# Performance work log

Measured on AMD Instinct MI355X. Metric: run time of the kernel, lower is better.

Reference implementation:

```python
import jax, jax.numpy as jnp
import numpy as np

HIDDEN = 1024
NUM_HEADS = 16
HEAD_DIM = HIDDEN // NUM_HEADS
EPS = 1e-12


def _layernorm(x, g, b):
    mu = jnp.mean(x, axis=-1, keepdims=True)
    var = jnp.var(x, axis=-1, keepdims=True)
    return (x - mu) * jax.lax.rsqrt(var + EPS) * g + b


def _attention(q, k, v, mask, Wd, bd, ln_g, ln_b):
    # q: [B,T,H], k/v: [B,S,H], mask: [B,1,1,S] additive
    B, T, _ = q.shape
    S = k.shape[1]
    qh = q.reshape(B, T, NUM_HEADS, HEAD_DIM).transpose(0, 2, 1, 3)  # [B,h,T,d]
    kh = k.reshape(B, S, NUM_HEADS, HEAD_DIM).transpose(0, 2, 1, 3)
    vh = v.reshape(B, S, NUM_HEADS, HEAD_DIM).transpose(0, 2, 1, 3)
    scores = jnp.einsum('bhtd,bhsd->bhts', qh, kh) / jnp.sqrt(jnp.float32(HEAD_DIM))
    if mask is not None:
        scores = scores + mask
    probs = jax.nn.softmax(scores, axis=-1)  # dropout = identity in eval
    ctx = jnp.einsum('bhts,bhsd->bthd', probs, vh)  # [B,T,h,d]
    # torch: w = dense.weight.t().view(h, d, H); einsum('bfnd,ndh->bfh')
    w = Wd.T.reshape(NUM_HEADS, HEAD_DIM, HIDDEN)
    proj = jnp.einsum('bthd,hdH->btH', ctx, w) + bd
    # residual is the (projected) query tensor q, per source
    return _layernorm(q + proj, ln_g, ln_b)


def setup_inputs() -> dict:
    key = jax.random.key(0)
    ks = jax.random.split(key, 12)
    s = 0.02
    B, S, T = 4, 1024, 1024
    return {
        'encoder_states': jax.random.normal(ks[0], (B, S, HIDDEN), jnp.float32),
        'decoder_inputs': jax.random.normal(ks[1], (B, T, HIDDEN), jnp.float32),
        'src_attention_mask': jnp.zeros((B, 1, 1, S), jnp.float32),
        'tgt_attention_mask': jnp.zeros((B, 1, 1, T), jnp.float32),
        'Wq': jax.random.normal(ks[2], (HIDDEN, HIDDEN), jnp.float32) * s,
        'bq': jnp.zeros((HIDDEN,), jnp.float32),
        'Wk': jax.random.normal(ks[3], (HIDDEN, HIDDEN), jnp.float32) * s,
        'bk': jnp.zeros((HIDDEN,), jnp.float32),
        'Wv': jax.random.normal(ks[4], (HIDDEN, HIDDEN), jnp.float32) * s,
        'bv': jnp.zeros((HIDDEN,), jnp.float32),
        'Wd': jax.random.normal(ks[5], (HIDDEN, HIDDEN), jnp.float32) * s,
        'bd': jnp.zeros((HIDDEN,), jnp.float32),
        'ln_g': jnp.ones((HIDDEN,), jnp.float32),
        'ln_b': jnp.zeros((HIDDEN,), jnp.float32),
    }


def reference(encoder_states, decoder_inputs, src_attention_mask, tgt_attention_mask,
              Wq, bq, Wk, bk, Wv, bv, Wd, bd, ln_g, ln_b):
    # projections (torch Linear: x @ W.T + b)
    q1 = decoder_inputs @ Wq.T + bq
    k1 = decoder_inputs @ Wk.T + bk
    v1 = decoder_inputs @ Wv.T + bv
    ek = encoder_states @ Wk.T + bk
    ev = encoder_states @ Wv.T + bv
    # self-attention over decoder states
    self_out = _attention(q1, k1, v1, tgt_attention_mask, Wd, bd, ln_g, ln_b)
    # cross-attention: query = self_out directly (no extra projection, per source)
    out = _attention(self_out, ek, ev, src_attention_mask, Wd, bd, ln_g, ln_b)
    return out
```

## Files before the change

kernel.cpp:

```cpp
#include <hip/hip_runtime.h>
#include <stdint.h>


#define B_   4
#define T_   1024
#define S_   1024
#define H_   1024
#define LOG2E 1.44269504088896340736f
#define SCALE_K (0.125f * LOG2E)

typedef __attribute__((ext_vector_type(8)))  __bf16       bf16x8;
typedef __attribute__((ext_vector_type(4)))  float        f32x4;
typedef __attribute__((ext_vector_type(16))) float        f32x16;
typedef __attribute__((ext_vector_type(4)))  unsigned int uint4v;

static __device__ __forceinline__ float bf2f(unsigned int u) {
    return __builtin_bit_cast(float, u << 16);
}
static __device__ __forceinline__ unsigned short f2bf(float f) {
    unsigned int x = __builtin_bit_cast(unsigned int, f);
    return (unsigned short)((x + 0x7fffu + ((x >> 16) & 1u)) >> 16);
}
static __device__ __forceinline__ unsigned int cvt_pk_bf16(float lo, float hi) {
    unsigned int r;
    asm("v_cvt_pk_bf16_f32 %0, %1, %2" : "=v"(r) : "v"(lo), "v"(hi));
    return r;
}
static __device__ __forceinline__ void perm32swap(unsigned int& a, unsigned int& b) {
    asm("v_permlane32_swap_b32 %0, %1" : "+v"(a), "+v"(b));
}
static __device__ __forceinline__ f32x4 mfma16(bf16x8 a, bf16x8 b, f32x4 c) {
    return __builtin_amdgcn_mfma_f32_16x16x32_bf16(a, b, c, 0, 0, 0);
}
static __device__ __forceinline__ f32x16 mfma32(bf16x8 a, bf16x8 b, f32x16 c) {
    return __builtin_amdgcn_mfma_f32_32x32x16_bf16(a, b, c, 0, 0, 0);
}

typedef const __attribute__((address_space(1))) void gv_t;
typedef __attribute__((address_space(3))) void lv_t;
static __device__ __forceinline__ void g2lds16(const void* g, void* l) {
    __builtin_amdgcn_global_load_lds((gv_t*)(size_t)g, (lv_t*)(unsigned int)(size_t)l, 16, 0, 0);
}

struct CvtArgs {
    const float* src[6];
    unsigned short* dst[6];
    float scale[6];
    int n4[6];
};
__global__ __launch_bounds__(256)
void cvt_multi(CvtArgs a) {
    const int k = blockIdx.y;
    const int i = blockIdx.x * 256 + threadIdx.x;
    if (i >= a.n4[k]) return;
    const float s = a.scale[k];
    float4 v = ((const float4*)a.src[k])[i];
    uint2 o;
    o.x = (unsigned)f2bf(v.x * s) | ((unsigned)f2bf(v.y * s) << 16);
    o.y = (unsigned)f2bf(v.z * s) | ((unsigned)f2bf(v.w * s) << 16);
    ((uint2*)a.dst[k])[i] = o;
}

struct GemmJob {
    const unsigned short* A[5];
    const unsigned short* W[5];
    const float* bias[5];
    float bs[5];
    unsigned short* O[5];
};
__global__ __launch_bounds__(256, 2)
void gemm_bf16(GemmJob job)
{
    __shared__ char smem[32768];
    char* As = smem;
    char* Bs = smem + 16384;
    const int tid = threadIdx.x;
    const int lane = tid & 63;
    const int w = tid >> 6;
    const int c = lane & 15, g = lane >> 4;
    const int wm = (w >> 1) * 64, wn = (w & 1) * 64;
    const int m0 = blockIdx.x * 128;
    const int set = blockIdx.y >> 3;
    const int n0 = (blockIdx.y & 7) * 128;
    const unsigned short* A    = job.A[set];
    const unsigned short* W    = job.W[set];
    const float* bias          = job.bias[set];
    const float bscale         = job.bs[set];
    unsigned short* O          = job.O[set];

    f32x4 acc[4][4];
#pragma unroll
    for (int i = 0; i < 4; i++)
#pragma unroll
        for (int j = 0; j < 4; j++) acc[i][j] = (f32x4){0.f, 0.f, 0.f, 0.f};

    const int srow = w * 32 + (lane >> 3);
    const int swzc = ((lane & 7) ^ (lane >> 3)) * 8;
    const unsigned short* gA = A + (size_t)(m0 + srow) * 1024 + swzc;
    const unsigned short* gB = W + (size_t)(n0 + srow) * 1024 + swzc;
    char* lA = As + w * 4096;
    char* lB = Bs + w * 4096;

    for (int kk = 0; kk < 1024; kk += 64) {
#pragma unroll
        for (int q = 0; q < 4; q++) {
            g2lds16(gA + kk + q*8192, lA + q*1024);
            g2lds16(gB + kk + q*8192, lB + q*1024);
        }
        __syncthreads();
#pragma unroll
        for (int ksub = 0; ksub < 2; ksub++) {
            bf16x8 af[4], bfr[4];
#pragma unroll
            for (int t = 0; t < 4; t++) {
                const int ra = wm + t*16 + c;
                const int rb = wn + t*16 + c;
                const int so = ((ksub*4 + g) ^ (c & 7)) << 4;
                af[t]  = *(const bf16x8*)(As + ra*128 + so);
                bfr[t] = *(const bf16x8*)(Bs + rb*128 + so);
            }
#pragma unroll
            for (int i = 0; i < 4; i++)
#pragma unroll
                for (int j = 0; j < 4; j++)
                    acc[i][j] = mfma16(af[i], bfr[j], acc[i][j]);
        }
        __syncthreads();
    }

    float bvv[4];
#pragma unroll
    for (int j = 0; j < 4; j++) bvv[j] = bias[n0 + wn + j*16 + c] * bscale;
    char* eb = As + w * 4096;
#pragma unroll
    for (int p = 0; p < 2; p++) {
#pragma unroll
        for (int ii = 0; ii < 2; ii++) {
            const int i = p*2 + ii;
#pragma unroll
            for (int j = 0; j < 4; j++)
#pragma unroll
                for (int r = 0; r < 4; r++)
                    *(unsigned short*)(eb + (ii*16 + g*4 + r)*128 + (c + j*16)*2)
                        = f2bf(acc[i][j][r] + bvv[j]);
        }
        asm volatile("s_waitcnt lgkmcnt(0)" ::: "memory");
#pragma unroll
        for (int it = 0; it < 4; it++) {
            const int lrow = it*8 + (lane >> 3);
            uint4 vv = *(const uint4*)(eb + lrow*128 + (lane & 7)*16);
            *(uint4*)(O + (size_t)(m0 + wm + p*32 + lrow)*1024 + n0 + wn + (lane & 7)*8) = vv;
        }
        if (p == 0) asm volatile("s_waitcnt lgkmcnt(0)" ::: "memory");
    }
}

__global__ __launch_bounds__(256)
void transpose_v(const unsigned short* __restrict__ V, unsigned short* __restrict__ VT)
{
    __shared__ char sm[8192];
    const int tid = threadIdx.x;
    const int bh = blockIdx.y, b = bh >> 4, h = bh & 15;
    const int s0 = blockIdx.x * 64;
    for (int u = tid; u < 512; u += 256) {
        const int r = u >> 3, sg = u & 7;
        uint4 v = *(const uint4*)(V + (size_t)(b*S_ + s0 + r)*H_ + h*64 + sg*8);
        *(uint4*)(sm + r*128 + ((sg*16) ^ ((r & 7) << 4))) = v;
    }
    __syncthreads();
    const int d = tid >> 2, ss = tid & 3;
    unsigned int ow[8];
#pragma unroll
    for (int j2 = 0; j2 < 8; j2++) {
        const int s_a = ss*16 + 2*j2, s_b = s_a + 1;
        unsigned int ta = *(const unsigned short*)(sm + s_a*128 + ((2*d) ^ ((s_a & 7) << 4)));
        unsigned int tb = *(const unsigned short*)(sm + s_b*128 + ((2*d) ^ ((s_b & 7) << 4)));
        ow[j2] = ta | (tb << 16);
    }
    unsigned short* op = VT + (size_t)(bh*64 + d)*S_ + s0 + ss*16;
    uint4 o0, o1;
    o0.x = ow[0]; o0.y = ow[1]; o0.z = ow[2]; o0.w = ow[3];
    o1.x = ow[4]; o1.y = ow[5]; o1.z = ow[6]; o1.w = ow[7];
    *(uint4*)op = o0;
    *(uint4*)(op + 8) = o1;
}

__global__ __launch_bounds__(256, 4)
void attn_fused2(const unsigned short* __restrict__ Q,
                 const unsigned short* __restrict__ Kx,
                 const unsigned short* __restrict__ VT,
                 const float* __restrict__ mask,
                 unsigned short* __restrict__ Octx)
{
    __shared__ char smem[32768 + 4096 + 512 + 16];
    float* mb   = (float*)(smem + 32768);
    float* lbuf = (float*)(smem + 32768 + 4096);
    int* flag   = (int*)(smem + 32768 + 4096 + 512);

    const int tid = threadIdx.x;
    const int lane = tid & 63, w = tid >> 6;
    const int qc = lane & 31, hi = lane >> 5;
    const int bh = blockIdx.y, b = bh >> 4, h = bh & 15;
    const int q0 = blockIdx.x * 128 + w * 32;

    const int r0 = tid >> 3, sg = tid & 7;
    const unsigned short* gK0 = Kx + (size_t)(b*S_ + r0)*H_  + h*64 + sg*8;
    const unsigned short* gK1 = gK0 + (size_t)32*H_;
    const unsigned short* gV0 = VT + (size_t)(bh*64 + r0)*S_ + sg*8;
    const unsigned short* gV1 = gV0 + (size_t)32*S_;
    const int woff = r0*128 + ((sg*16) ^ ((r0 & 7) << 4));

    const unsigned short* qptr = Q + (size_t)(b*T_ + q0 + qc)*H_ + h*64 + hi*8;
    bf16x8 qf[4];
#pragma unroll
    for (int s = 0; s < 4; s++) qf[s] = *(const bf16x8*)(qptr + s*16);

    uint4 cK0 = *(const uint4*)gK0;
    uint4 cK1 = *(const uint4*)gK1;
    uint4 cV0 = *(const uint4*)gV0;
    uint4 cV1 = *(const uint4*)gV1;

    if (tid == 0) *flag = 0;
    __syncthreads();
    {
        float4 mv = ((const float4*)(mask + (size_t)b*S_))[tid];
        float4 ms;
        ms.x = mv.x * LOG2E; ms.y = mv.y * LOG2E; ms.z = mv.z * LOG2E; ms.w = mv.w * LOG2E;
        ((float4*)mb)[tid] = ms;
        if (mv.x != 0.f || mv.y != 0.f || mv.z != 0.f || mv.w != 0.f) atomicOr(flag, 1);
    }
    {
        char* b0 = smem;
        *(uint4*)(b0 + woff)               = cK0;
        *(uint4*)(b0 + 4096 + woff)        = cK1;
        *(uint4*)(b0 + 8192 + woff)        = cV0;
        *(uint4*)(b0 + 8192 + 4096 + woff) = cV1;
    }
    __syncthreads();
    const int msk = *flag;

    f32x16 o0 = {}, o1 = {};
    float lacc = 0.f;

    for (int t = 0; t < 16; ++t) {
        uint4 nK0, nK1, nV0, nV1;
        if (t < 15) {
            const size_t ko = (size_t)(t + 1) * 64 * H_;
            const int    vo = (t + 1) * 64;
            nK0 = *(const uint4*)(gK0 + ko);
            nK1 = *(const uint4*)(gK1 + ko);
            nV0 = *(const uint4*)(gV0 + vo);
            nV1 = *(const uint4*)(gV1 + vo);
        }
        char* Ks = smem + (t & 1) * 16384;
        char* Vs = Ks + 8192;

#pragma unroll
        for (int ts = 0; ts < 2; ++ts) {
            f32x16 st = {};
            __builtin_amdgcn_s_setprio(1);
#pragma unroll
            for (int step = 0; step < 4; ++step) {
                bf16x8 ak = *(const bf16x8*)(Ks + (ts*32 + qc)*128 +
                             ((step*32 + hi*16) ^ ((qc & 7) << 4)));
                st = mfma32(ak, qf[step], st);
            }
            __builtin_amdgcn_s_setprio(0);

            float pv[16];
            if (msk) {
#pragma unroll
                for (int rq = 0; rq < 4; ++rq) {
                    const float4 bb = *(const float4*)(mb + t*64 + ts*32 + rq*8 + hi*4);
#pragma unroll
                    for (int e = 0; e < 4; ++e)
                        pv[rq*4 + e] = __builtin_amdgcn_exp2f(st[rq*4 + e] + (&bb.x)[e]);
                }
            } else {
#pragma unroll
                for (int r = 0; r < 16; ++r) pv[r] = __builtin_amdgcn_exp2f(st[r]);
            }
#pragma unroll
            for (int r = 0; r < 16; ++r) lacc += pv[r];

#pragma unroll
            for (int half = 0; half < 2; ++half) {
                unsigned w0 = cvt_pk_bf16(pv[half*8 + 0], pv[half*8 + 1]);
                unsigned w1 = cvt_pk_bf16(pv[half*8 + 2], pv[half*8 + 3]);
                unsigned w2 = cvt_pk_bf16(pv[half*8 + 4], pv[half*8 + 5]);
                unsigned w3 = cvt_pk_bf16(pv[half*8 + 6], pv[half*8 + 7]);
                perm32swap(w0, w2);
                perm32swap(w1, w3);
                uint4v fw; fw[0] = w0; fw[1] = w1; fw[2] = w2; fw[3] = w3;
                const bf16x8 pa = __builtin_bit_cast(bf16x8, fw);
                const int scol = (ts*64 + half*32 + hi*16) ^ ((qc & 7) << 4);
                bf16x8 v0 = *(const bf16x8*)(Vs + qc*128        + scol);
                bf16x8 v1 = *(const bf16x8*)(Vs + (32 + qc)*128 + scol);
                __builtin_amdgcn_s_setprio(1);
                o0 = mfma32(pa, v0, o0);
                o1 = mfma32(pa, v1, o1);
                __builtin_amdgcn_s_setprio(0);
            }
        }

        if (t < 15) {
            char* nxt = smem + ((t + 1) & 1) * 16384;
            *(uint4*)(nxt + woff)               = nK0;
            *(uint4*)(nxt + 4096 + woff)        = nK1;
            *(uint4*)(nxt + 8192 + woff)        = nV0;
            *(uint4*)(nxt + 8192 + 4096 + woff) = nV1;
        }
        __syncthreads();
    }

    {
        unsigned la = __builtin_bit_cast(unsigned, lacc);
        unsigned lb = la;
        perm32swap(la, lb);
        const float ltot = __builtin_bit_cast(float, la) + __builtin_bit_cast(float, lb);
        const float linv = 1.f / ltot;
        if (hi == 0) lbuf[w*32 + qc] = linv;
    }
    __syncthreads();
    float4 li[4];
#pragma unroll
    for (int rq = 0; rq < 4; ++rq)
        li[rq] = *(const float4*)(lbuf + w*32 + rq*8 + hi*4);

#pragma unroll
    for (int dt = 0; dt < 2; ++dt) {
        const f32x16& oo = dt ? o1 : o0;
#pragma unroll
        for (int r = 0; r < 16; ++r) {
            const int qrow = (r & 3) + 8*(r >> 2) + 4*hi;
            const float val = oo[r] * (&li[r >> 2].x)[r & 3];
            Octx[(size_t)(b*T_ + q0 + qrow)*H_ + h*64 + dt*32 + qc] = f2bf(val);
        }
    }
}

template<int OUTMODE>
__global__ __launch_bounds__(256)
void ln_kernel(const unsigned short* __restrict__ resid,
               const unsigned short* __restrict__ proj,
               const float* __restrict__ gam,
               const float* __restrict__ bet,
               unsigned short* __restrict__ obf,
               float* __restrict__ of32)
{
    __shared__ float red[8];
    const int tid = threadIdx.x;
    const int lane = tid & 63, w = tid >> 6;
    const int i = tid * 4;
    const size_t base = (size_t)blockIdx.x * 1024 + i;
    uint2 rv = *(const uint2*)(resid + base);
    uint2 pv = *(const uint2*)(proj + base);
    float x[4];
    x[0] = bf2f(rv.x & 0xffffu) + bf2f(pv.x & 0xffffu);
    x[1] = bf2f(rv.x >> 16)     + bf2f(pv.x >> 16);
    x[2] = bf2f(rv.y & 0xffffu) + bf2f(pv.y & 0xffffu);
    x[3] = bf2f(rv.y >> 16)     + bf2f(pv.y >> 16);
    float s = x[0] + x[1] + x[2] + x[3];
    float q = x[0]*x[0] + x[1]*x[1] + x[2]*x[2] + x[3]*x[3];
#pragma unroll
    for (int off = 1; off < 64; off <<= 1) {
        s += __shfl_xor(s, off);
        q += __shfl_xor(q, off);
    }
    if (lane == 0) { red[w*2] = s; red[w*2 + 1] = q; }
    __syncthreads();
    s = red[0] + red[2] + red[4] + red[6];
    q = red[1] + red[3] + red[5] + red[7];
    const float mu   = s * (1.f/1024.f);
    const float var  = q * (1.f/1024.f) - mu*mu;
    const float rstd = rsqrtf(var + 1e-12f);
    const float4 gv = *(const float4*)(gam + i);
    const float4 bv = *(const float4*)(bet + i);
    float y[4];
#pragma unroll
    for (int j = 0; j < 4; j++)
        y[j] = (x[j] - mu) * rstd * (&gv.x)[j] + (&bv.x)[j];
    if (OUTMODE == 0) {
        uint2 oo;
        oo.x = (unsigned)f2bf(y[0]) | ((unsigned)f2bf(y[1]) << 16);
        oo.y = (unsigned)f2bf(y[2]) | ((unsigned)f2bf(y[3]) << 16);
        *(uint2*)(obf + base) = oo;
    } else {
        float4 oo; oo.x = y[0]; oo.y = y[1]; oo.z = y[2]; oo.w = y[3];
        *(float4*)(of32 + base) = oo;
    }
}

extern "C" void kernel_launch(void* const* d_in, const int* in_sizes, int n_in,
                              void* d_out, int out_size, void* d_ws, size_t ws_size,
                              hipStream_t stream)
{
    const float* enc   = (const float*)d_in[0];
    const float* dec   = (const float*)d_in[1];
    const float* smask = (const float*)d_in[2];
    const float* tmask = (const float*)d_in[3];
    const float* Wq = (const float*)d_in[4];
    const float* bq = (const float*)d_in[5];
    const float* Wk = (const float*)d_in[6];
    const float* bk = (const float*)d_in[7];
    const float* Wv = (const float*)d_in[8];
    const float* bv = (const float*)d_in[9];
    const float* Wd = (const float*)d_in[10];
    const float* bd = (const float*)d_in[11];
    const float* lng = (const float*)d_in[12];
    const float* lnb = (const float*)d_in[13];
    float* out = (float*)d_out;

    char* ws = (char*)d_ws;
    const size_t MB = 1024ull * 1024ull;
    unsigned short* dec_bf = (unsigned short*)(ws + 0*MB);
    unsigned short* enc_bf = (unsigned short*)(ws + 8*MB);
    unsigned short* Wq_bf  = (unsigned short*)(ws + 16*MB);
    unsigned short* Wk_bf  = (unsigned short*)(ws + 18*MB);
    unsigned short* Wv_bf  = (unsigned short*)(ws + 20*MB);
    unsigned short* Wd_bf  = (unsigned short*)(ws + 22*MB);
    unsigned short* q1  = (unsigned short*)(ws + 24*MB);
    unsigned short* k1  = (unsigned short*)(ws + 32*MB);
    unsigned short* v1  = (unsigned short*)(ws + 40*MB);
    unsigned short* ek  = (unsigned short*)(ws + 48*MB);
    unsigned short* ev  = (unsigned short*)(ws + 56*MB);
    unsigned short* vt1 = (unsigned short*)(ws + 64*MB);
    unsigned short* ctx      = dec_bf;
    unsigned short* proj     = enc_bf;
    unsigned short* self_out = k1;
    unsigned short* evt      = v1;

    CvtArgs ca;
    ca.src[0] = dec; ca.dst[0] = dec_bf; ca.scale[0] = 1.f;      ca.n4[0] = 1048576;
    ca.src[1] = enc; ca.dst[1] = enc_bf; ca.scale[1] = 1.f;      ca.n4[1] = 1048576;
    ca.src[2] = Wq;  ca.dst[2] = Wq_bf;  ca.scale[2] = 1.f;      ca.n4[2] = 262144;
    ca.src[3] = Wk;  ca.dst[3] = Wk_bf;  ca.scale[3] = SCALE_K;  ca.n4[3] = 262144;
    ca.src[4] = Wv;  ca.dst[4] = Wv_bf;  ca.scale[4] = 1.f;      ca.n4[4] = 262144;
    ca.src[5] = Wd;  ca.dst[5] = Wd_bf;  ca.scale[5] = 1.f;      ca.n4[5] = 262144;
    cvt_multi<<<dim3(4096, 6), 256, 0, stream>>>(ca);

    GemmJob j1;
    j1.A[0] = dec_bf; j1.W[0] = Wq_bf; j1.bias[0] = bq; j1.bs[0] = 1.f;     j1.O[0] = q1;
    j1.A[1] = dec_bf; j1.W[1] = Wk_bf; j1.bias[1] = bk; j1.bs[1] = SCALE_K; j1.O[1] = k1;
    j1.A[2] = dec_bf; j1.W[2] = Wv_bf; j1.bias[2] = bv; j1.bs[2] = 1.f;     j1.O[2] = v1;
    j1.A[3] = enc_bf; j1.W[3] = Wk_bf; j1.bias[3] = bk; j1.bs[3] = SCALE_K; j1.O[3] = ek;
    j1.A[4] = enc_bf; j1.W[4] = Wv_bf; j1.bias[4] = bv; j1.bs[4] = 1.f;     j1.O[4] = ev;
    gemm_bf16<<<dim3(32, 40), 256, 0, stream>>>(j1);

    transpose_v<<<dim3(16, 64), 256, 0, stream>>>(v1, vt1);
    transpose_v<<<dim3(16, 64), 256, 0, stream>>>(ev, evt);

    GemmJob jd;
    for (int i = 0; i < 5; i++) {
        jd.A[i] = ctx; jd.W[i] = Wd_bf; jd.bias[i] = bd; jd.bs[i] = 1.f; jd.O[i] = proj;
    }

    attn_fused2<<<dim3(8, 64), 256, 0, stream>>>(q1, k1, vt1, tmask, ctx);
    gemm_bf16<<<dim3(32, 8), 256, 0, stream>>>(jd);
    ln_kernel<0><<<4096, 256, 0, stream>>>(q1, proj, lng, lnb, self_out, nullptr);

    attn_fused2<<<dim3(8, 64), 256, 0, stream>>>(self_out, ek, evt, smask, ctx);
    gemm_bf16<<<dim3(32, 8), 256, 0, stream>>>(jd);
    ln_kernel<1><<<4096, 256, 0, stream>>>(self_out, proj, lng, lnb, nullptr, out);
}
```

Measured before the change: 176.4 us.

## Use direct global-to-LDS loads and MFMA row-sum in attention kernel

The attention kernel now stages K and V tiles with direct global-to-LDS loads (g2lds16) instead of loading into registers and storing to shared memory. That frees registers and removes the LDS store step at the end of each iteration. The softmax denominator is computed by an extra MFMA against a ones vector rather than by scalar accumulation, a cross-lane swap and an extra LDS pass with a barrier. Both score tiles are computed before the exponentials, and the two V transposes are merged into one launch. The trade-off is an additional MFMA per PV step and a per-element division at the end.

```diff
diff --git a/kernel.cpp b/kernel.cpp
--- a/kernel.cpp
+++ b/kernel.cpp
@@ -156,9 +156,12 @@
 }
 
 __global__ __launch_bounds__(256)
-void transpose_v(const unsigned short* __restrict__ V, unsigned short* __restrict__ VT)
+void transpose_v2(const unsigned short* __restrict__ V0, unsigned short* __restrict__ VT0,
+                  const unsigned short* __restrict__ V1, unsigned short* __restrict__ VT1)
 {
     __shared__ char sm[8192];
+    const unsigned short* V = blockIdx.z ? V1 : V0;
+    unsigned short* VT      = blockIdx.z ? VT1 : VT0;
     const int tid = threadIdx.x;
     const int bh = blockIdx.y, b = bh >> 4, h = bh & 15;
     const int s0 = blockIdx.x * 64;
@@ -186,16 +189,15 @@
 }
 
 __global__ __launch_bounds__(256, 4)
-void attn_fused2(const unsigned short* __restrict__ Q,
+void attn_fused3(const unsigned short* __restrict__ Q,
                  const unsigned short* __restrict__ Kx,
                  const unsigned short* __restrict__ VT,
                  const float* __restrict__ mask,
                  unsigned short* __restrict__ Octx)
 {
-    __shared__ char smem[32768 + 4096 + 512 + 16];
-    float* mb   = (float*)(smem + 32768);
-    float* lbuf = (float*)(smem + 32768 + 4096);
-    int* flag   = (int*)(smem + 32768 + 4096 + 512);
+    __shared__ char smem[32768 + 4096 + 16];
+    float* mb = (float*)(smem + 32768);
+    int* flag = (int*)(smem + 32768 + 4096);
 
     const int tid = threadIdx.x;
     const int lane = tid & 63, w = tid >> 6;
@@ -203,24 +205,27 @@
     const int bh = blockIdx.y, b = bh >> 4, h = bh & 15;
     const int q0 = blockIdx.x * 128 + w * 32;
 
-    const int r0 = tid >> 3, sg = tid & 7;
-    const unsigned short* gK0 = Kx + (size_t)(b*S_ + r0)*H_  + h*64 + sg*8;
-    const unsigned short* gK1 = gK0 + (size_t)32*H_;
-    const unsigned short* gV0 = VT + (size_t)(bh*64 + r0)*S_ + sg*8;
-    const unsigned short* gV1 = gV0 + (size_t)32*S_;
-    const int woff = r0*128 + ((sg*16) ^ ((r0 & 7) << 4));
+    const int rs = tid >> 3, sg = tid & 7;
+    const int scol = (sg ^ (rs & 7)) * 8;
+    const unsigned short* gK = Kx + (size_t)(b*S_ + rs)*H_ + h*64 + scol;
+    const unsigned short* gV = VT + (size_t)(bh*64 + rs)*S_ + scol;
+    char* ldK = smem + w * 1024;
+    char* ldV = smem + 8192 + w * 1024;
 
     const unsigned short* qptr = Q + (size_t)(b*T_ + q0 + qc)*H_ + h*64 + hi*8;
     bf16x8 qf[4];
 #pragma unroll
     for (int s = 0; s < 4; s++) qf[s] = *(const bf16x8*)(qptr + s*16);
 
-    uint4 cK0 = *(const uint4*)gK0;
-    uint4 cK1 = *(const uint4*)gK1;
-    uint4 cV0 = *(const uint4*)gV0;
-    uint4 cV1 = *(const uint4*)gV1;
+    uint4v onesw;
+    onesw[0] = 0x3f803f80u; onesw[1] = 0x3f803f80u; onesw[2] = 0x3f803f80u; onesw[3] = 0x3f803f80u;
+    const bf16x8 ones = __builtin_bit_cast(bf16x8, onesw);
 
     if (tid == 0) *flag = 0;
+    g2lds16(gK,           ldK);
+    g2lds16(gK + 32*H_,   ldK + 4096);
+    g2lds16(gV,           ldV);
+    g2lds16(gV + 32*S_,   ldV + 4096);
     __syncthreads();
     {
         float4 mv = ((const float4*)(mask + (size_t)b*S_))[tid];
@@ -229,103 +234,76 @@
         ((float4*)mb)[tid] = ms;
         if (mv.x != 0.f || mv.y != 0.f || mv.z != 0.f || mv.w != 0.f) atomicOr(flag, 1);
     }
-    {
-        char* b0 = smem;
-        *(uint4*)(b0 + woff)               = cK0;
-        *(uint4*)(b0 + 4096 + woff)        = cK1;
-        *(uint4*)(b0 + 8192 + woff)        = cV0;
-        *(uint4*)(b0 + 8192 + 4096 + woff) = cV1;
-    }
     __syncthreads();
     const int msk = *flag;
 
-    f32x16 o0 = {}, o1 = {};
-    float lacc = 0.f;
+    f32x16 o0 = {}, o1 = {}, lsum = {};
 
     for (int t = 0; t < 16; ++t) {
-        uint4 nK0, nK1, nV0, nV1;
         if (t < 15) {
+            const int nb = (t + 1) & 1;
             const size_t ko = (size_t)(t + 1) * 64 * H_;
             const int    vo = (t + 1) * 64;
-            nK0 = *(const uint4*)(gK0 + ko);
-            nK1 = *(const uint4*)(gK1 + ko);
-            nV0 = *(const uint4*)(gV0 + vo);
-            nV1 = *(const uint4*)(gV1 + vo);
-        }
-        char* Ks = smem + (t & 1) * 16384;
-        char* Vs = Ks + 8192;
+            g2lds16(gK + ko,          ldK + nb*16384);
+            g2lds16(gK + ko + 32*H_,  ldK + nb*16384 + 4096);
+            g2lds16(gV + vo,          ldV + nb*16384);
+            g2lds16(gV + vo + 32*S_,  ldV + nb*16384 + 4096);
+        }
+        const char* Ks = smem + (t & 1) * 16384;
+        const char* Vs = Ks + 8192;
+
+        f32x16 st0 = {}, st1 = {};
+        __builtin_amdgcn_s_setprio(1);
+#pragma unroll
+        for (int step = 0; step < 4; ++step) {
+            bf16x8 ak = *(const bf16x8*)(Ks + qc*128 + ((step*32 + hi*16) ^ ((qc & 7) << 4)));
+            st0 = mfma32(ak, qf[step], st0);
+        }
+#pragma unroll
+        for (int step = 0; step < 4; ++step) {
+            bf16x8 ak = *(const bf16x8*)(Ks + (32 + qc)*128 + ((step*32 + hi*16) ^ ((qc & 7) << 4)));
+            st1 = mfma32(ak, qf[step], st1);
+        }
+        __builtin_amdgcn_s_setprio(0);
 
 #pragma unroll
         for (int ts = 0; ts < 2; ++ts) {
-            f32x16 st = {};
-            __builtin_amdgcn_s_setprio(1);
-#pragma unroll
-            for (int step = 0; step < 4; ++step) {
-                bf16x8 ak = *(const bf16x8*)(Ks + (ts*32 + qc)*128 +
-                             ((step*32 + hi*16) ^ ((qc & 7) << 4)));
-                st = mfma32(ak, qf[step], st);
-            }
-            __builtin_amdgcn_s_setprio(0);
-
-            float pv[16];
+            f32x16& st = ts ? st1 : st0;
             if (msk) {
 #pragma unroll
                 for (int rq = 0; rq < 4; ++rq) {
                     const float4 bb = *(const float4*)(mb + t*64 + ts*32 + rq*8 + hi*4);
 #pragma unroll
                     for (int e = 0; e < 4; ++e)
-                        pv[rq*4 + e] = __builtin_amdgcn_exp2f(st[rq*4 + e] + (&bb.x)[e]);
+                        st[rq*4 + e] = __builtin_amdgcn_exp2f(st[rq*4 + e] + (&bb.x)[e]);
                 }
             } else {
 #pragma unroll
-                for (int r = 0; r < 16; ++r) pv[r] = __builtin_amdgcn_exp2f(st[r]);
+                for (int r = 0; r < 16; ++r) st[r] = __builtin_amdgcn_exp2f(st[r]);
             }
-#pragma unroll
-            for (int r = 0; r < 16; ++r) lacc += pv[r];
 
 #pragma unroll
             for (int half = 0; half < 2; ++half) {
-                unsigned w0 = cvt_pk_bf16(pv[half*8 + 0], pv[half*8 + 1]);
-                unsigned w1 = cvt_pk_bf16(pv[half*8 + 2], pv[half*8 + 3]);
-                unsigned w2 = cvt_pk_bf16(pv[half*8 + 4], pv[half*8 + 5]);
-                unsigned w3 = cvt_pk_bf16(pv[half*8 + 6], pv[half*8 + 7]);
+                unsigned w0 = cvt_pk_bf16(st[half*8 + 0], st[half*8 + 1]);
+                unsigned w1 = cvt_pk_bf16(st[half*8 + 2], st[half*8 + 3]);
+                unsigned w2 = cvt_pk_bf16(st[half*8 + 4], st[half*8 + 5]);
+                unsigned w3 = cvt_pk_bf16(st[half*8 + 6], st[half*8 + 7]);
                 perm32swap(w0, w2);
                 perm32swap(w1, w3);
                 uint4v fw; fw[0] = w0; fw[1] = w1; fw[2] = w2; fw[3] = w3;
                 const bf16x8 pa = __builtin_bit_cast(bf16x8, fw);
-                const int scol = (ts*64 + half*32 + hi*16) ^ ((qc & 7) << 4);
-                bf16x8 v0 = *(const bf16x8*)(Vs + qc*128        + scol);
-                bf16x8 v1 = *(const bf16x8*)(Vs + (32 + qc)*128 + scol);
+                const int vcol = (ts*64 + half*32 + hi*16) ^ ((qc & 7) << 4);
+                bf16x8 v0 = *(const bf16x8*)(Vs + qc*128        + vcol);
+                bf16x8 v1 = *(const bf16x8*)(Vs + (32 + qc)*128 + vcol);
                 __builtin_amdgcn_s_setprio(1);
-                o0 = mfma32(pa, v0, o0);
-                o1 = mfma32(pa, v1, o1);
+                o0   = mfma32(pa, v0,   o0);
+                o1   = mfma32(pa, v1,   o1);
+                lsum = mfma32(pa, ones, lsum);
                 __builtin_amdgcn_s_setprio(0);
             }
         }
-
-        if (t < 15) {
-            char* nxt = smem + ((t + 1) & 1) * 16384;
-            *(uint4*)(nxt + woff)               = nK0;
-            *(uint4*)(nxt + 4096 + woff)        = nK1;
-            *(uint4*)(nxt + 8192 + woff)        = nV0;
-            *(uint4*)(nxt + 8192 + 4096 + woff) = nV1;
-        }
         __syncthreads();
     }
-
-    {
-        unsigned la = __builtin_bit_cast(unsigned, lacc);
-        unsigned lb = la;
-        perm32swap(la, lb);
-        const float ltot = __builtin_bit_cast(float, la) + __builtin_bit_cast(float, lb);
-        const float linv = 1.f / ltot;
-        if (hi == 0) lbuf[w*32 + qc] = linv;
-    }
-    __syncthreads();
-    float4 li[4];
-#pragma unroll
-    for (int rq = 0; rq < 4; ++rq)
-        li[rq] = *(const float4*)(lbuf + w*32 + rq*8 + hi*4);
 
 #pragma unroll
     for (int dt = 0; dt < 2; ++dt) {
@@ -333,7 +311,7 @@
 #pragma unroll
         for (int r = 0; r < 16; ++r) {
             const int qrow = (r & 3) + 8*(r >> 2) + 4*hi;
-            const float val = oo[r] * (&li[r >> 2].x)[r & 3];
+            const float val = oo[r] / lsum[r];
             Octx[(size_t)(b*T_ + q0 + qrow)*H_ + h*64 + dt*32 + qc] = f2bf(val);
         }
     }
@@ -447,19 +425,18 @@
     j1.A[4] = enc_bf; j1.W[4] = Wv_bf; j1.bias[4] = bv; j1.bs[4] = 1.f;     j1.O[4] = ev;
     gemm_bf16<<<dim3(32, 40), 256, 0, stream>>>(j1);
 
-    transpose_v<<<dim3(16, 64), 256, 0, stream>>>(v1, vt1);
-    transpose_v<<<dim3(16, 64), 256, 0, stream>>>(ev, evt);
+    transpose_v2<<<dim3(16, 64, 2), 256, 0, stream>>>(v1, vt1, ev, evt);
 
     GemmJob jd;
     for (int i = 0; i < 5; i++) {
         jd.A[i] = ctx; jd.W[i] = Wd_bf; jd.bias[i] = bd; jd.bs[i] = 1.f; jd.O[i] = proj;
     }
 
-    attn_fused2<<<dim3(8, 64), 256, 0, stream>>>(q1, k1, vt1, tmask, ctx);
+    attn_fused3<<<dim3(8, 64), 256, 0, stream>>>(q1, k1, vt1, tmask, ctx);
     gemm_bf16<<<dim3(32, 8), 256, 0, stream>>>(jd);
     ln_kernel<0><<<4096, 256, 0, stream>>>(q1, proj, lng, lnb, self_out, nullptr);
 
-    attn_fused2<<<dim3(8, 64), 256, 0, stream>>>(self_out, ek, evt, smask, ctx);
+    attn_fused3<<<dim3(8, 64), 256, 0, stream>>>(self_out, ek, evt, smask, ctx);
     gemm_bf16<<<dim3(32, 8), 256, 0, stream>>>(jd);
     ln_kernel<1><<<4096, 256, 0, stream>>>(self_out, proj, lng, lnb, nullptr, out);
 }
```

Measured after the change: 183.1 us. +3.8%, slower.
